# Kernel tuning notes

Hardware: AMD Instinct MI355X
Metric: run time of the kernel (lower is better)

Reference implementation:

```python
import jax, jax.numpy as jnp
import numpy as np

B, S, D, F = 4, 4096, 1024, 256


def _ln(x, g, b, eps=1e-5):
    m = x.mean(-1, keepdims=True)
    v = ((x - m) ** 2).mean(-1, keepdims=True)
    return (x - m) / jnp.sqrt(v + eps) * g + b


def setup_inputs() -> dict:
    key = jax.random.key(0)
    ks = jax.random.split(key, 8)
    return {
        "x": jax.random.normal(ks[0], (B, S, D), jnp.float32),
        "W_to": jax.random.normal(ks[1], (2 * F, D), jnp.float32) * 0.02,   # to_spectral.weight [out,in]
        "log_decay": jnp.zeros((F,), jnp.float32),
        "frequencies": jax.random.normal(ks[2], (F,), jnp.float32) * 0.01,
        "W_from": jax.random.normal(ks[3], (D, 2 * F), jnp.float32) * 0.02,  # from_spectral.weight
        "ln1_g": jnp.ones((D,), jnp.float32), "ln1_b": jnp.zeros((D,), jnp.float32),
        "ln3_g": jnp.ones((D,), jnp.float32), "ln3_b": jnp.zeros((D,), jnp.float32),
        "W_ffn1": jax.random.normal(ks[4], (4 * D, D), jnp.float32) * 0.02,
        "b_ffn1": jnp.zeros((4 * D,), jnp.float32),
        "W_ffn2": jax.random.normal(ks[5], (D, 4 * D), jnp.float32) * 0.02,
        "b_ffn2": jnp.zeros((D,), jnp.float32),
    }


def reference(x, W_to, log_decay, frequencies, W_from, ln1_g, ln1_b,
              ln3_g, ln3_b, W_ffn1, b_ffn1, W_ffn2, b_ffn2):
    Bc, Sc, Dc = x.shape
    Fc = log_decay.shape[0]
    dt = 1.0  # registered buffer dt = 1.0

    residual = x
    h = _ln(x, ln1_g, ln1_b)
    spec = jnp.einsum('bsd,fd->bsf', h, W_to)          # [B,S,2F]
    real, imag = spec[..., :Fc], spec[..., Fc:]

    decay = jax.nn.sigmoid(log_decay)                   # [F]
    omega = jnp.tanh(frequencies) * 0.1
    c, s = jnp.cos(omega * dt), jnp.sin(omega * dt)

    def step(carry, u):
        sr, si = carry
        r, i = u                                        # [B,F]
        sr = sr * decay + r * 0.1
        si = si * decay + i * 0.1
        nr = jnp.clip(sr * c - si * s, -10.0, 10.0)
        ni = jnp.clip(sr * s + si * c, -10.0, 10.0)
        return (nr, ni), (nr, ni)

    init = (jnp.zeros((Bc, Fc), x.dtype), jnp.zeros((Bc, Fc), x.dtype))
    _, (out_r, out_i) = jax.lax.scan(
        step, init, (real.transpose(1, 0, 2), imag.transpose(1, 0, 2)))
    spectral_out = jnp.concatenate(
        [out_r.transpose(1, 0, 2), out_i.transpose(1, 0, 2)], axis=-1)  # [B,S,2F]

    h = jnp.einsum('bsf,df->bsd', spectral_out, W_from)
    x2 = residual + h * 0.1

    # FFN block (dropout = identity in eval)
    r3 = x2
    h = _ln(x2, ln3_g, ln3_b)
    h = jnp.einsum('bsd,ed->bse', h, W_ffn1) + b_ffn1
    h = jax.nn.gelu(h, approximate=False)               # nn.GELU default = exact erf
    h = jnp.einsum('bse,de->bsd', h, W_ffn2) + b_ffn2
    return r3 + h * 0.1
```

## Files before the change

### kernel.cpp

```cpp
#include <hip/hip_runtime.h>
#include <hip/hip_bf16.h>
#include <math.h>

typedef _Float16 f16x8 __attribute__((ext_vector_type(8)));
typedef _Float16 f16x4 __attribute__((ext_vector_type(4)));
typedef float f32x4 __attribute__((ext_vector_type(4)));
typedef float f32x16 __attribute__((ext_vector_type(16)));
typedef int v4i __attribute__((ext_vector_type(4)));
typedef int v8i __attribute__((ext_vector_type(8)));

#define GAS __attribute__((address_space(1)))
#define LAS __attribute__((address_space(3)))

__device__ __forceinline__ void async_load16(const void* g, void* l) {
  __builtin_amdgcn_global_load_lds((const GAS void*)g, (LAS void*)l, 16, 0, 0);
}

__device__ __forceinline__ float fast_gelu(float x) {
  float x3 = x * x * x;
  float u = 0.7978845608f * x + 0.0356774081f * x3;
  float e = __expf(2.0f * u);
  float t = 1.0f - 2.0f / (e + 1.0f);
  return 0.5f * x * (1.0f + t);
}

__device__ __forceinline__ int pack4_fp8(float a, float b, float c, float d) {
  int p = __builtin_amdgcn_cvt_pk_fp8_f32(a, b, 0, false);
  p = __builtin_amdgcn_cvt_pk_fp8_f32(c, d, p, true);
  return p;
}

__global__ __launch_bounds__(256) void cvt_all_kernel(
    const float* __restrict__ W_to, const float* __restrict__ W_from,
    const float* __restrict__ W_ffn1, const float* __restrict__ W_ffn2,
    _Float16* __restrict__ Wto_h, _Float16* __restrict__ Wfrom_h,
    unsigned char* __restrict__ Wf1_8, unsigned char* __restrict__ Wf2_8) {
  int id = blockIdx.x * 256 + threadIdx.x;
  if (id < 131072) {
    int i = id * 4;
    float4 v = *(const float4*)(W_to + i);
    f16x4 o;
    o.x = (_Float16)v.x; o.y = (_Float16)v.y; o.z = (_Float16)v.z; o.w = (_Float16)v.w;
    *(f16x4*)(Wto_h + i) = o;
  } else if (id < 262144) {
    int i = (id - 131072) * 4;
    float4 v = *(const float4*)(W_from + i);
    f16x4 o;
    o.x = (_Float16)v.x; o.y = (_Float16)v.y; o.z = (_Float16)v.z; o.w = (_Float16)v.w;
    *(f16x4*)(Wfrom_h + i) = o;
  } else if (id < 1310720) {
    int i = (id - 262144) * 4;
    float4 v = *(const float4*)(W_ffn1 + i);
    *(int*)(Wf1_8 + i) = pack4_fp8(v.x, v.y, v.z, v.w);
  } else {
    int id2 = id - 1310720;
    int n = id2 >> 10;
    int p0 = (id2 & 1023) * 4;
    int p7 = p0 & 127;
    int grp = (p7 >> 2) & 3;
    int h = (p7 >> 4) & 1;
    int k_src = (p0 & ~127) | (p7 & 96) | (grp << 3) | (h << 2);
    float4 v = *(const float4*)(W_ffn2 + (size_t)n * 4096 + k_src);
    *(int*)(Wf2_8 + (size_t)n * 4096 + p0) = pack4_fp8(v.x, v.y, v.z, v.w);
  }
}

template <int OUT8>
__global__ __launch_bounds__(256) void ln_kernel(const float* __restrict__ x,
                                                 const float* __restrict__ gamma,
                                                 const float* __restrict__ beta,
                                                 _Float16* __restrict__ outH,
                                                 unsigned char* __restrict__ outB) {
  int row = blockIdx.x;
  int t = threadIdx.x;
  float4 v = ((const float4*)(x + (size_t)row * 1024))[t];
  float s = v.x + v.y + v.z + v.w;
  float s2 = v.x * v.x + v.y * v.y + v.z * v.z + v.w * v.w;
#pragma unroll
  for (int o = 32; o > 0; o >>= 1) { s += __shfl_xor(s, o); s2 += __shfl_xor(s2, o); }
  __shared__ float red[8];
  int w = t >> 6;
  if ((t & 63) == 0) { red[w] = s; red[4 + w] = s2; }
  __syncthreads();
  s = red[0] + red[1] + red[2] + red[3];
  s2 = red[4] + red[5] + red[6] + red[7];
  float mean = s * (1.0f / 1024.0f);
  float var = s2 * (1.0f / 1024.0f) - mean * mean;
  float rstd = rsqrtf(var + 1e-5f);
  float4 gv = ((const float4*)gamma)[t];
  float4 bv = ((const float4*)beta)[t];
  float y0 = (v.x - mean) * rstd * gv.x + bv.x;
  float y1 = (v.y - mean) * rstd * gv.y + bv.y;
  float y2 = (v.z - mean) * rstd * gv.z + bv.z;
  float y3 = (v.w - mean) * rstd * gv.w + bv.w;
  if (OUT8) {
    *(int*)(outB + (size_t)row * 1024 + t * 4) = pack4_fp8(y0, y1, y2, y3);
  } else {
    f16x4 o;
    o.x = (_Float16)y0; o.y = (_Float16)y1; o.z = (_Float16)y2; o.w = (_Float16)y3;
    *(f16x4*)(outH + (size_t)row * 1024 + t * 4) = o;
  }
}

#define SCAN_CH 64
#define SCAN_W 64
__global__ __launch_bounds__(256) void scan_kernel(const _Float16* __restrict__ spec,
                                                   const float* __restrict__ log_decay,
                                                   const float* __restrict__ freq,
                                                   _Float16* __restrict__ so) {
  const int S = 4096;
  const int nchunks = S / SCAN_CH;
  int f = threadIdx.x;
  int b = blockIdx.x / nchunks;
  int ck = blockIdx.x % nchunks;
  int t0 = ck * SCAN_CH;
  int ts = (ck == 0) ? 0 : (t0 - SCAN_W);
  int nsteps = t0 + SCAN_CH - ts;

  float decay = 1.0f / (1.0f + expf(-log_decay[f]));
  float om = tanhf(freq[f]) * 0.1f;
  float co = cosf(om);
  float sn = sinf(om);
  float sr = 0.0f, si = 0.0f;

  const _Float16* base = spec + (size_t)b * S * 512;
  _Float16* ob = so + (size_t)b * S * 512;

  float rb[8], ib[8];
#pragma unroll
  for (int j = 0; j < 8; j++) {
    rb[j] = (float)base[(size_t)(ts + j) * 512 + f];
    ib[j] = (float)base[(size_t)(ts + j) * 512 + 256 + f];
  }
  for (int gs = 0; gs < nsteps; gs += 8) {
    float cr[8], ci[8];
#pragma unroll
    for (int j = 0; j < 8; j++) { cr[j] = rb[j]; ci[j] = ib[j]; }
    if (gs + 8 < nsteps) {
      int nx = ts + gs + 8;
#pragma unroll
      for (int j = 0; j < 8; j++) {
        rb[j] = (float)base[(size_t)(nx + j) * 512 + f];
        ib[j] = (float)base[(size_t)(nx + j) * 512 + 256 + f];
      }
    }
#pragma unroll
    for (int j = 0; j < 8; j++) {
      int t = ts + gs + j;
      sr = sr * decay + cr[j] * 0.1f;
      si = si * decay + ci[j] * 0.1f;
      float nr = sr * co - si * sn;
      float ni = sr * sn + si * co;
      nr = fminf(10.0f, fmaxf(-10.0f, nr));
      ni = fminf(10.0f, fmaxf(-10.0f, ni));
      sr = nr; si = ni;
      if (t >= t0) {
        ob[(size_t)t * 512 + f] = (_Float16)nr;
        ob[(size_t)t * 512 + 256 + f] = (_Float16)ni;
      }
    }
  }
}

template <int EPI>
__global__ __launch_bounds__(256, 2) void gemm_nt_kernel(
    const _Float16* __restrict__ A, const _Float16* __restrict__ Bm,
    const float* __restrict__ bias, const float* resid,
    float* outF, _Float16* __restrict__ outH,
    int M, int N, int K, int lda, int ldb) {
  __shared__ __align__(16) _Float16 As[2][128 * 32];
  __shared__ __align__(16) _Float16 Bs[2][128 * 32];
  const int tid = threadIdx.x;
  const int lane = tid & 63;
  const int wave = tid >> 6;
  const int wm = (wave >> 1) * 64;
  const int wn = (wave & 1) * 64;
  const int bm = blockIdx.x * 128;
  const int bn = blockIdx.y * 128;

  size_t ga[2], gb[2];
  int lo[2];
#pragma unroll
  for (int rep = 0; rep < 2; rep++) {
    int lsi = tid + rep * 256;
    int row = lsi >> 2;
    int slot = lsi & 3;
    int sw = (row ^ (row >> 2)) & 3;
    int gseg = slot ^ sw;
    lo[rep] = lsi * 8;
    ga[rep] = (size_t)(bm + row) * lda + (size_t)gseg * 8;
    gb[rep] = (size_t)(bn + row) * ldb + (size_t)gseg * 8;
  }

  const int q = lane >> 4;
  const int ml = lane & 15;
  int aaddr[4], baddr[4];
#pragma unroll
  for (int i = 0; i < 4; i++) {
    int r = wm + i * 16 + ml;
    aaddr[i] = (r * 4 + (q ^ ((r ^ (r >> 2)) & 3))) * 8;
    int rn = wn + i * 16 + ml;
    baddr[i] = (rn * 4 + (q ^ ((rn ^ (rn >> 2)) & 3))) * 8;
  }

  const f32x4 zero = {0.0f, 0.0f, 0.0f, 0.0f};
  f32x4 acc[4][4];
#pragma unroll
  for (int i = 0; i < 4; i++)
#pragma unroll
    for (int j = 0; j < 4; j++) acc[i][j] = zero;

  for (int k0 = 0; k0 < K; k0 += 64) {
    __syncthreads();
#pragma unroll
    for (int h = 0; h < 2; h++) {
#pragma unroll
      for (int rep = 0; rep < 2; rep++) {
        async_load16(A + ga[rep] + k0 + h * 32, &As[h][lo[rep]]);
        async_load16(Bm + gb[rep] + k0 + h * 32, &Bs[h][lo[rep]]);
      }
    }
    __syncthreads();
#pragma unroll
    for (int h = 0; h < 2; h++) {
      f16x8 af[4], bf[4];
#pragma unroll
      for (int i = 0; i < 4; i++) {
        af[i] = *(const f16x8*)(As[h] + aaddr[i]);
        bf[i] = *(const f16x8*)(Bs[h] + baddr[i]);
      }
#pragma unroll
      for (int i = 0; i < 4; i++)
#pragma unroll
        for (int j = 0; j < 4; j++)
          acc[i][j] = __builtin_amdgcn_mfma_f32_16x16x32_f16(bf[j], af[i], acc[i][j], 0, 0, 0);
    }
  }

#pragma unroll
  for (int i = 0; i < 4; i++) {
    int gm = bm + wm + i * 16 + ml;
#pragma unroll
    for (int j = 0; j < 4; j++) {
      int gn = bn + wn + j * 16 + q * 4;
      size_t idx = (size_t)gm * N + gn;
      f32x4 c = acc[i][j];
      if (EPI == 0) {
        f16x4 o;
        o.x = (_Float16)c[0]; o.y = (_Float16)c[1];
        o.z = (_Float16)c[2]; o.w = (_Float16)c[3];
        *(f16x4*)(outH + idx) = o;
      } else {
        float4 rv = *(const float4*)(resid + idx);
        float4 bv = bias ? *(const float4*)(bias + gn) : float4{0.f, 0.f, 0.f, 0.f};
        float4 o;
        o.x = rv.x + 0.1f * (c[0] + bv.x);
        o.y = rv.y + 0.1f * (c[1] + bv.y);
        o.z = rv.z + 0.1f * (c[2] + bv.z);
        o.w = rv.w + 0.1f * (c[3] + bv.w);
        *(float4*)(outF + idx) = o;
      }
    }
  }
}

template <int EPI>
__global__ __launch_bounds__(512, 1) void gemm_fp8_kernel(
    const unsigned char* __restrict__ A, const unsigned char* __restrict__ Bm,
    const float* __restrict__ bias, const float* resid,
    float* outF, unsigned char* __restrict__ outB,
    int M, int N, int K, int lda, int ldb) {
  __shared__ __align__(16) unsigned char As[4][256 * 64];
  __shared__ __align__(16) unsigned char Bs[4][256 * 64];
  const int tid = threadIdx.x;
  const int lane = tid & 63;
  const int wave = tid >> 6;
  const int wm = (wave >> 2) * 128;
  const int wn = (wave & 3) * 64;
  const int bm = blockIdx.x * 256;
  const int bn = blockIdx.y * 256;

  size_t ga[2], gb[2];
  int lo[2];
#pragma unroll
  for (int rep = 0; rep < 2; rep++) {
    int lsi = tid + rep * 512;
    int row = lsi >> 2;
    int slot = lsi & 3;
    int sw = (row ^ (row >> 2)) & 3;
    int gseg = slot ^ sw;
    lo[rep] = lsi * 16;
    ga[rep] = (size_t)(bm + row) * lda + (size_t)gseg * 16;
    gb[rep] = (size_t)(bn + row) * ldb + (size_t)gseg * 16;
  }

  const int ml = lane & 31;
  const int h2 = lane >> 5;
  int aaddr[4][2], baddr[2][2];
#pragma unroll
  for (int i = 0; i < 4; i++) {
    int r = wm + i * 32 + ml;
    int sw = (r ^ (r >> 2)) & 3;
    aaddr[i][0] = (r * 4 + ((2 * h2) ^ sw)) * 16;
    aaddr[i][1] = (r * 4 + ((2 * h2 + 1) ^ sw)) * 16;
  }
#pragma unroll
  for (int j = 0; j < 2; j++) {
    int rn = wn + j * 32 + ml;
    int sw = (rn ^ (rn >> 2)) & 3;
    baddr[j][0] = (rn * 4 + ((2 * h2) ^ sw)) * 16;
    baddr[j][1] = (rn * 4 + ((2 * h2 + 1) ^ sw)) * 16;
  }

  f32x16 acc[4][2];
#pragma unroll
  for (int i = 0; i < 4; i++)
#pragma unroll
    for (int j = 0; j < 2; j++)
#pragma unroll
      for (int r = 0; r < 16; r++) acc[i][j][r] = 0.0f;

  const int NT = K >> 6;

#define STAGE_T(s, t)                                                       \
  {                                                                         \
    _Pragma("unroll")                                                       \
    for (int rep = 0; rep < 2; rep++) {                                     \
      async_load16(A + ga[rep] + (size_t)(t) * 64, &As[s][lo[rep]]);        \
      async_load16(Bm + gb[rep] + (size_t)(t) * 64, &Bs[s][lo[rep]]);       \
    }                                                                       \
  }

#define COMPUTE_T(s)                                                        \
  {                                                                         \
    v8i af[4], bf[2];                                                       \
    _Pragma("unroll")                                                       \
    for (int i = 0; i < 4; i++) {                                           \
      v4i* ap = (v4i*)&af[i];                                               \
      ap[0] = *(const v4i*)(As[s] + aaddr[i][0]);                           \
      ap[1] = *(const v4i*)(As[s] + aaddr[i][1]);                           \
    }                                                                       \
    _Pragma("unroll")                                                       \
    for (int j = 0; j < 2; j++) {                                           \
      v4i* bp = (v4i*)&bf[j];                                               \
      bp[0] = *(const v4i*)(Bs[s] + baddr[j][0]);                           \
      bp[1] = *(const v4i*)(Bs[s] + baddr[j][1]);                           \
    }                                                                       \
    __builtin_amdgcn_s_setprio(1);                                          \
    _Pragma("unroll")                                                       \
    for (int i = 0; i < 4; i++) {                                           \
      _Pragma("unroll")                                                     \
      for (int j = 0; j < 2; j++)                                           \
        acc[i][j] = __builtin_amdgcn_mfma_scale_f32_32x32x64_f8f6f4(        \
            bf[j], af[i], acc[i][j], 0, 0, 0, 0x7F7F7F7F, 0, 0x7F7F7F7F);   \
    }                                                                       \
    __builtin_amdgcn_s_setprio(0);                                          \
  }

#define SYNC_T(vmc)                                                         \
  asm volatile("s_waitcnt vmcnt(" #vmc ") lgkmcnt(0)" ::: "memory");        \
  __builtin_amdgcn_sched_barrier(0);                                        \
  __builtin_amdgcn_s_barrier();

  STAGE_T(0, 0)
  STAGE_T(1, 1)
  STAGE_T(2, 2)
  SYNC_T(8)

  for (int t4 = 0; t4 + 8 <= NT; t4 += 4) {
#pragma unroll
    for (int u = 0; u < 4; u++) {
      STAGE_T((u + 3) & 3, t4 + u + 3)
      COMPUTE_T(u)
      SYNC_T(8)
    }
  }

  STAGE_T(3, NT - 1)
  COMPUTE_T(0)
  SYNC_T(8)
  COMPUTE_T(1)
  SYNC_T(4)
  COMPUTE_T(2)
  SYNC_T(0)
  COMPUTE_T(3)

#undef STAGE_T
#undef COMPUTE_T
#undef SYNC_T

#pragma unroll
  for (int i = 0; i < 4; i++) {
    int gm = bm + wm + i * 32 + ml;
#pragma unroll
    for (int j = 0; j < 2; j++) {
      if (EPI == 2) {
        int w[4];
#pragma unroll
        for (int grp = 0; grp < 4; grp++) {
          int n0 = bn + wn + j * 32 + grp * 8 + h2 * 4;
          float4 bv = *(const float4*)(bias + n0);
          float v0 = fast_gelu(acc[i][j][grp * 4 + 0] + bv.x);
          float v1 = fast_gelu(acc[i][j][grp * 4 + 1] + bv.y);
          float v2 = fast_gelu(acc[i][j][grp * 4 + 2] + bv.z);
          float v3 = fast_gelu(acc[i][j][grp * 4 + 3] + bv.w);
          w[grp] = pack4_fp8(v0, v1, v2, v3);
        }
        int pbase = bn + wn + j * 32 + h2 * 16;
        v4i pk = {w[0], w[1], w[2], w[3]};
        *(v4i*)(outB + (size_t)gm * N + pbase) = pk;
      } else {
#pragma unroll
        for (int grp = 0; grp < 4; grp++) {
          int n0 = bn + wn + j * 32 + grp * 8 + h2 * 4;
          size_t idx = (size_t)gm * N + n0;
          float4 rv = *(const float4*)(resid + idx);
          float4 bv = *(const float4*)(bias + n0);
          float4 o;
          o.x = rv.x + 0.1f * (acc[i][j][grp * 4 + 0] + bv.x);
          o.y = rv.y + 0.1f * (acc[i][j][grp * 4 + 1] + bv.y);
          o.z = rv.z + 0.1f * (acc[i][j][grp * 4 + 2] + bv.z);
          o.w = rv.w + 0.1f * (acc[i][j][grp * 4 + 3] + bv.w);
          *(float4*)(outF + idx) = o;
        }
      }
    }
  }
}

extern "C" void kernel_launch(void* const* d_in, const int* in_sizes, int n_in,
                              void* d_out, int out_size, void* d_ws, size_t ws_size,
                              hipStream_t stream) {
  const int Bb = 4, S = 4096, D = 1024, F = 256;
  const int M = Bb * S;
  const int N1 = 2 * F;
  const int NF = 4 * D;

  const float* x       = (const float*)d_in[0];
  const float* W_to    = (const float*)d_in[1];
  const float* log_dec = (const float*)d_in[2];
  const float* freq    = (const float*)d_in[3];
  const float* W_from  = (const float*)d_in[4];
  const float* ln1_g   = (const float*)d_in[5];
  const float* ln1_b   = (const float*)d_in[6];
  const float* ln3_g   = (const float*)d_in[7];
  const float* ln3_b   = (const float*)d_in[8];
  const float* W_ffn1  = (const float*)d_in[9];
  const float* b_ffn1  = (const float*)d_in[10];
  const float* W_ffn2  = (const float*)d_in[11];
  const float* b_ffn2  = (const float*)d_in[12];
  float* out = (float*)d_out;
  (void)in_sizes; (void)n_in; (void)out_size; (void)ws_size;

  char* ws = (char*)d_ws;
  _Float16*      Wto_h   = (_Float16*)(ws);
  _Float16*      Wfrom_h = (_Float16*)(ws + (size_t)1048576);
  unsigned char* Wf1_8   = (unsigned char*)(ws + (size_t)2097152);
  unsigned char* Wf2_8   = (unsigned char*)(ws + (size_t)6291456);
  char* dyn = ws + (size_t)10485760;
  _Float16*      h16     = (_Float16*)(dyn);
  _Float16*      so      = (_Float16*)(dyn);
  _Float16*      spec16  = (_Float16*)(dyn + (size_t)33554432);
  unsigned char* h8      = (unsigned char*)(dyn + (size_t)50331648);
  unsigned char* g8      = (unsigned char*)(dyn + (size_t)67108864);

  cvt_all_kernel<<<9216, 256, 0, stream>>>(W_to, W_from, W_ffn1, W_ffn2,
                                           Wto_h, Wfrom_h, Wf1_8, Wf2_8);

  ln_kernel<0><<<M, 256, 0, stream>>>(x, ln1_g, ln1_b, h16, nullptr);

  gemm_nt_kernel<0><<<dim3(M / 128, N1 / 128), 256, 0, stream>>>(
      h16, Wto_h, nullptr, nullptr, nullptr, spec16, M, N1, D, D, D);

  scan_kernel<<<Bb * (S / SCAN_CH), 256, 0, stream>>>(spec16, log_dec, freq, so);

  gemm_nt_kernel<1><<<dim3(M / 128, D / 128), 256, 0, stream>>>(
      so, Wfrom_h, nullptr, x, out, nullptr, M, D, N1, N1, N1);

  ln_kernel<1><<<M, 256, 0, stream>>>(out, ln3_g, ln3_b, nullptr, h8);

  gemm_fp8_kernel<2><<<dim3(M / 256, NF / 256), 512, 0, stream>>>(
      h8, Wf1_8, b_ffn1, nullptr, nullptr, g8, M, NF, D, D, D);

  gemm_fp8_kernel<1><<<dim3(M / 256, D / 256), 512, 0, stream>>>(
      g8, Wf2_8, b_ffn2, out, out, nullptr, M, D, NF, NF, NF);
}
```

Measured before the change: 502.9 us.

## Use 128x128 single-buffered fp8 GEMM for FFN1, tweak 256 kernel loads

Adds a new 128x128-tile fp8 MFMA GEMM with 256 threads and up to 3 blocks per CU, and uses it for the FFN1+GELU GEMM. The old 256x256 multi-stage kernel is renamed and kept for FFN2. That kernel now loads A fragments per row-tile right before use, which cuts register pressure, and it drops the sched_barrier. The new kernel has no software pipelining: it uses two syncthreads per K step and no overlap. It relies on occupancy to hide latency, and smaller tiles bring less data reuse per block.

```diff
diff --git a/kernel.cpp b/kernel.cpp
--- a/kernel.cpp
+++ b/kernel.cpp
@@ -265,7 +265,133 @@
 }
 
 template <int EPI>
-__global__ __launch_bounds__(512, 1) void gemm_fp8_kernel(
+__global__ __launch_bounds__(256, 3) void gemm_fp8_kernel(
+    const unsigned char* __restrict__ A, const unsigned char* __restrict__ Bm,
+    const float* __restrict__ bias, const float* resid,
+    float* outF, unsigned char* __restrict__ outB,
+    int M, int N, int K, int lda, int ldb) {
+  __shared__ __align__(16) unsigned char As[2][128 * 64];
+  __shared__ __align__(16) unsigned char Bs[2][128 * 64];
+  const int tid = threadIdx.x;
+  const int lane = tid & 63;
+  const int wave = tid >> 6;
+  const int wm = (wave >> 1) * 64;
+  const int wn = (wave & 1) * 64;
+  const int bm = blockIdx.x * 128;
+  const int bn = blockIdx.y * 128;
+
+  size_t ga[2], gb[2];
+  int lo[2];
+#pragma unroll
+  for (int rep = 0; rep < 2; rep++) {
+    int lsi = tid + rep * 256;
+    int row = lsi >> 2;
+    int slot = lsi & 3;
+    int sw = (row ^ (row >> 2)) & 3;
+    int gseg = slot ^ sw;
+    lo[rep] = lsi * 16;
+    ga[rep] = (size_t)(bm + row) * lda + (size_t)gseg * 16;
+    gb[rep] = (size_t)(bn + row) * ldb + (size_t)gseg * 16;
+  }
+
+  const int ml = lane & 31;
+  const int h2 = lane >> 5;
+  int aaddr[2][2], baddr[2][2];
+#pragma unroll
+  for (int t = 0; t < 2; t++) {
+    int r = wm + t * 32 + ml;
+    int sw = (r ^ (r >> 2)) & 3;
+    aaddr[t][0] = (r * 4 + ((2 * h2) ^ sw)) * 16;
+    aaddr[t][1] = (r * 4 + ((2 * h2 + 1) ^ sw)) * 16;
+    int rn = wn + t * 32 + ml;
+    int swn = (rn ^ (rn >> 2)) & 3;
+    baddr[t][0] = (rn * 4 + ((2 * h2) ^ swn)) * 16;
+    baddr[t][1] = (rn * 4 + ((2 * h2 + 1) ^ swn)) * 16;
+  }
+
+  f32x16 acc[2][2];
+#pragma unroll
+  for (int i = 0; i < 2; i++)
+#pragma unroll
+    for (int j = 0; j < 2; j++)
+#pragma unroll
+      for (int r = 0; r < 16; r++) acc[i][j][r] = 0.0f;
+
+  for (int k0 = 0; k0 < K; k0 += 128) {
+    __syncthreads();
+#pragma unroll
+    for (int h = 0; h < 2; h++) {
+#pragma unroll
+      for (int rep = 0; rep < 2; rep++) {
+        async_load16(A + ga[rep] + k0 + h * 64, &As[h][lo[rep]]);
+        async_load16(Bm + gb[rep] + k0 + h * 64, &Bs[h][lo[rep]]);
+      }
+    }
+    __syncthreads();
+#pragma unroll
+    for (int h = 0; h < 2; h++) {
+      const unsigned char* Ab = As[h];
+      const unsigned char* Bb = Bs[h];
+      v8i af[2], bf[2];
+#pragma unroll
+      for (int tt = 0; tt < 2; tt++) {
+        v4i a0 = *(const v4i*)(Ab + aaddr[tt][0]);
+        v4i a1 = *(const v4i*)(Ab + aaddr[tt][1]);
+        af[tt] = __builtin_shufflevector(a0, a1, 0, 1, 2, 3, 4, 5, 6, 7);
+        v4i b0 = *(const v4i*)(Bb + baddr[tt][0]);
+        v4i b1 = *(const v4i*)(Bb + baddr[tt][1]);
+        bf[tt] = __builtin_shufflevector(b0, b1, 0, 1, 2, 3, 4, 5, 6, 7);
+      }
+#pragma unroll
+      for (int i = 0; i < 2; i++)
+#pragma unroll
+        for (int j = 0; j < 2; j++)
+          acc[i][j] = __builtin_amdgcn_mfma_scale_f32_32x32x64_f8f6f4(
+              bf[j], af[i], acc[i][j], 0, 0, 0, 0x7F7F7F7F, 0, 0x7F7F7F7F);
+    }
+  }
+
+#pragma unroll
+  for (int i = 0; i < 2; i++) {
+    int gm = bm + wm + i * 32 + ml;
+#pragma unroll
+    for (int j = 0; j < 2; j++) {
+      if (EPI == 2) {
+        int w[4];
+#pragma unroll
+        for (int grp = 0; grp < 4; grp++) {
+          int n0 = bn + wn + j * 32 + grp * 8 + h2 * 4;
+          float4 bv = *(const float4*)(bias + n0);
+          float v0 = fast_gelu(acc[i][j][grp * 4 + 0] + bv.x);
+          float v1 = fast_gelu(acc[i][j][grp * 4 + 1] + bv.y);
+          float v2 = fast_gelu(acc[i][j][grp * 4 + 2] + bv.z);
+          float v3 = fast_gelu(acc[i][j][grp * 4 + 3] + bv.w);
+          w[grp] = pack4_fp8(v0, v1, v2, v3);
+        }
+        int pbase = bn + wn + j * 32 + h2 * 16;
+        v4i pk = {w[0], w[1], w[2], w[3]};
+        *(v4i*)(outB + (size_t)gm * N + pbase) = pk;
+      } else {
+#pragma unroll
+        for (int grp = 0; grp < 4; grp++) {
+          int n0 = bn + wn + j * 32 + grp * 8 + h2 * 4;
+          size_t idx = (size_t)gm * N + n0;
+          float4 rv = *(const float4*)(resid + idx);
+          float4 bv = *(const float4*)(bias + n0);
+          float4 o;
+          o.x = rv.x + 0.1f * (acc[i][j][grp * 4 + 0] + bv.x);
+          o.y = rv.y + 0.1f * (acc[i][j][grp * 4 + 1] + bv.y);
+          o.z = rv.z + 0.1f * (acc[i][j][grp * 4 + 2] + bv.z);
+          o.w = rv.w + 0.1f * (acc[i][j][grp * 4 + 3] + bv.w);
+          *(float4*)(outF + idx) = o;
+        }
+      }
+    }
+  }
+}
+
+template <int EPI>
+__global__ __launch_bounds__(512, 1) void gemm_fp8_256_kernel(
     const unsigned char* __restrict__ A, const unsigned char* __restrict__ Bm,
     const float* __restrict__ bias, const float* resid,
     float* outF, unsigned char* __restrict__ outB,
@@ -333,13 +459,7 @@
 
 #define COMPUTE_T(s)                                                        \
   {                                                                         \
-    v8i af[4], bf[2];                                                       \
-    _Pragma("unroll")                                                       \
-    for (int i = 0; i < 4; i++) {                                           \
-      v4i* ap = (v4i*)&af[i];                                               \
-      ap[0] = *(const v4i*)(As[s] + aaddr[i][0]);                           \
-      ap[1] = *(const v4i*)(As[s] + aaddr[i][1]);                           \
-    }                                                                       \
+    v8i bf[2];                                                              \
     _Pragma("unroll")                                                       \
     for (int j = 0; j < 2; j++) {                                           \
       v4i* bp = (v4i*)&bf[j];                                               \
@@ -349,17 +469,20 @@
     __builtin_amdgcn_s_setprio(1);                                          \
     _Pragma("unroll")                                                       \
     for (int i = 0; i < 4; i++) {                                           \
-      _Pragma("unroll")                                                     \
-      for (int j = 0; j < 2; j++)                                           \
-        acc[i][j] = __builtin_amdgcn_mfma_scale_f32_32x32x64_f8f6f4(        \
-            bf[j], af[i], acc[i][j], 0, 0, 0, 0x7F7F7F7F, 0, 0x7F7F7F7F);   \
+      v8i af;                                                               \
+      v4i* ap = (v4i*)&af;                                                  \
+      ap[0] = *(const v4i*)(As[s] + aaddr[i][0]);                           \
+      ap[1] = *(const v4i*)(As[s] + aaddr[i][1]);                           \
+      acc[i][0] = __builtin_amdgcn_mfma_scale_f32_32x32x64_f8f6f4(          \
+          bf[0], af, acc[i][0], 0, 0, 0, 0x7F7F7F7F, 0, 0x7F7F7F7F);        \
+      acc[i][1] = __builtin_amdgcn_mfma_scale_f32_32x32x64_f8f6f4(          \
+          bf[1], af, acc[i][1], 0, 0, 0, 0x7F7F7F7F, 0, 0x7F7F7F7F);        \
     }                                                                       \
     __builtin_amdgcn_s_setprio(0);                                          \
   }
 
 #define SYNC_T(vmc)                                                         \
   asm volatile("s_waitcnt vmcnt(" #vmc ") lgkmcnt(0)" ::: "memory");        \
-  __builtin_amdgcn_sched_barrier(0);                                        \
   __builtin_amdgcn_s_barrier();
 
   STAGE_T(0, 0)
@@ -479,9 +602,9 @@
 
   ln_kernel<1><<<M, 256, 0, stream>>>(out, ln3_g, ln3_b, nullptr, h8);
 
-  gemm_fp8_kernel<2><<<dim3(M / 256, NF / 256), 512, 0, stream>>>(
+  gemm_fp8_kernel<2><<<dim3(M / 128, NF / 128), 256, 0, stream>>>(
       h8, Wf1_8, b_ffn1, nullptr, nullptr, g8, M, NF, D, D, D);
 
-  gemm_fp8_kernel<1><<<dim3(M / 256, D / 256), 512, 0, stream>>>(
+  gemm_fp8_256_kernel<1><<<dim3(M / 256, D / 256), 512, 0, stream>>>(
       g8, Wf2_8, b_ffn2, out, out, nullptr, M, D, NF, NF, NF);
 }
```

Measured after the change: 448.1 us (median of 2 runs). 1.12x faster.
